# Optimization experiments

Measured on AMD Instinct MI355X. Metric: run time of the kernel, lower is better.

## Reference

```python
import jax, jax.numpy as jnp
import numpy as np

EPS = 1e-5  # torch BatchNorm2d default eps


def _lin(x, W, b):
    # torch nn.Linear: y = x @ W.T + b, W is [out, in]
    return jnp.einsum('...i,oi->...o', x, W) + b


def _bn(x, g, b):
    # BatchNorm2d in training mode: normalize per channel (last axis here)
    # over all other axes (B, N, K) with biased variance.
    m = jnp.mean(x, axis=(0, 1, 2), keepdims=True)
    v = jnp.mean(jnp.square(x - m), axis=(0, 1, 2), keepdims=True)
    return (x - m) * jax.lax.rsqrt(v + EPS) * g + b


def _gelu(x):
    return jax.nn.gelu(x, approximate=False)  # torch F.gelu default is erf


def _knn_idx(points, k):
    # squared euclidean pairwise distances, then k smallest per query
    pn = jnp.sum(points * points, axis=-1)  # [B,N]
    d2 = pn[:, :, None] + pn[:, None, :] - 2.0 * jnp.einsum('bnd,bmd->bnm', points, points)
    _, idx = jax.lax.top_k(-d2, k)  # [B,N,k], nearest first (includes self)
    return idx


def _gather(x, idx):
    # x: [B,N,D], idx: [B,N,K] -> [B,N,K,D]
    return jax.vmap(lambda a, i: a[i])(x, idx)


def setup_inputs() -> dict:
    key = jax.random.key(0)
    ks = jax.random.split(key, 20)
    B, N, Dp, Df, k = 2, 8192, 3, 128, 16

    def lin_params(kw, kb, din, dout):
        s = 1.0 / np.sqrt(din)
        W = jax.random.uniform(kw, (dout, din), jnp.float32, -s, s)
        b = jax.random.uniform(kb, (dout,), jnp.float32, -s, s)
        return W, b

    Wq, bq = lin_params(ks[0], ks[1], Df, Df)
    Wk, bk = lin_params(ks[2], ks[3], Df, Df)
    Wv, bv = lin_params(ks[4], ks[5], Df, Df)
    Wd1, bd1 = lin_params(ks[6], ks[7], Dp, Dp)
    Wd2, bd2 = lin_params(ks[8], ks[9], Dp, Df)
    Wg1, bg1 = lin_params(ks[10], ks[11], Df, Df)
    Wg2, bg2 = lin_params(ks[12], ks[13], Df, Df)

    return {
        'feats': jax.random.normal(ks[14], (B, N, Df), jnp.float32),
        'points': jax.random.normal(ks[15], (B, N, Dp), jnp.float32),
        'Wq': Wq, 'bq': bq, 'Wk': Wk, 'bk': bk, 'Wv': Wv, 'bv': bv,
        'Wd1': Wd1, 'bd1': bd1, 'Wd2': Wd2, 'bd2': bd2,
        'Wg1': Wg1, 'bg1': bg1, 'Wg2': Wg2, 'bg2': bg2,
        'gd': jnp.ones((Dp,), jnp.float32), 'betad': jnp.zeros((Dp,), jnp.float32),
        'gg1': jnp.ones((Df,), jnp.float32), 'betag1': jnp.zeros((Df,), jnp.float32),
        'gg2': jnp.ones((Df,), jnp.float32), 'betag2': jnp.zeros((Df,), jnp.float32),
        'k': 16,
    }


def reference(feats, points, Wq, bq, Wk, bk, Wv, bv, Wd1, bd1, Wd2, bd2,
              Wg1, bg1, Wg2, bg2, gd, betad, gg1, betag1, gg2, betag2, k):
    idx = _knn_idx(points, k)                     # [B,N,k]
    knn_feats = _gather(feats, idx)               # [B,N,k,Df]
    knn_points = _gather(points, idx)             # [B,N,k,Dp]

    pos = points[:, :, None, :] - knn_points      # [B,N,k,Dp]
    pos = _lin(pos, Wd1, bd1)
    pos = _gelu(_bn(pos, gd, betad))
    pos = _lin(pos, Wd2, bd2)                     # [B,N,k,Df]

    q = _lin(feats, Wq, bq)                       # [B,N,Df]
    key_t = _lin(knn_feats, Wk, bk)               # [B,N,k,Df]
    gamma = q[:, :, None, :] - key_t + pos
    gamma = _gelu(_bn(gamma, gg1, betag1))
    gamma = _lin(gamma, Wg1, bg1)
    gamma = _gelu(_bn(gamma, gg2, betag2))
    gamma = _lin(gamma, Wg2, bg2)

    rho = jax.nn.softmax(gamma, axis=-2)          # softmax over k neighbors
    value = _lin(knn_feats, Wv, bv) + pos
    return jnp.einsum('bnkd,bnkd->bnd', rho, value)
```

## Files before the change

### kernel.cpp

```cpp
#include <hip/hip_runtime.h>
#include <hip/hip_bf16.h>
#include <math.h>

#define NPTS 8192
#define STAT_CNT 262144.0f
#define BN_EPS 1e-5f

typedef __attribute__((__ext_vector_type__(8))) __bf16 bf16x8;
typedef __attribute__((__ext_vector_type__(4))) float f32x4;

#define SD_SUM 0
#define SD_SSQ 4
#define SD_SC 8
#define SD_SH 12
#define SG1_SC 16
#define SG1_SH 144
#define SG2_SC 272
#define SG2_SH 400
#define PG1 528
#define PG2 8720
#define STATS_FLOATS 16912

__device__ __forceinline__ unsigned short f2b(float x){
  unsigned u = __float_as_uint(x);
  return (unsigned short)((u + 0x7FFFu + ((u>>16)&1u)) >> 16);
}
__device__ __forceinline__ float b2f(unsigned short h){
  return __uint_as_float(((unsigned)h)<<16);
}
__device__ __forceinline__ float gelu_f(float x){
  return 0.5f*x*(1.0f + erff(x*0.70710678118654752440f));
}
__device__ __forceinline__ int swz(int row, int byteInRow){
  return row*256 + (byteInRow ^ ((row&7)<<4));
}
__device__ __forceinline__ float dist2f(float qx,float qy,float qz,float qpn,
                                        float x,float y,float z,float w){
  return (qpn + w) - 2.0f*fmaf(qx,x,fmaf(qy,y,qz*z));
}

#define MFMA16(a,b,c) __builtin_amdgcn_mfma_f32_16x16x32_bf16((a),(b),(c),0,0,0)

__device__ __forceinline__ bf16x8 ldsA8(const unsigned short* sA, int row, int k){
  return *(const bf16x8*)((const char*)sA + swz(row, k*2));
}
__device__ __forceinline__ bf16x8 ldW8(const unsigned short* W, int n, int k){
  return *(const bf16x8*)(W + n*128 + k);
}

__device__ __forceinline__ void gemm32(f32x4 acc[2][8], const unsigned short* sA,
                                       const unsigned short* W, int row0, int lane){
  int r = lane & 15, g = lane >> 4;
  #pragma unroll
  for (int ks=0; ks<4; ++ks){
    int k = ks*32 + g*8;
    bf16x8 a0 = ldsA8(sA, row0 + r, k);
    bf16x8 a1 = ldsA8(sA, row0 + 16 + r, k);
    #pragma unroll
    for (int nt=0; nt<8; ++nt){
      bf16x8 b = ldW8(W, nt*16 + r, k);
      acc[0][nt] = MFMA16(a0, b, acc[0][nt]);
      acc[1][nt] = MFMA16(a1, b, acc[1][nt]);
    }
  }
}

__global__ __launch_bounds__(256) void k_prep(
    const float* __restrict__ feats, const float* __restrict__ Wq, const float* __restrict__ Wk,
    const float* __restrict__ Wv, const float* __restrict__ Wg1, const float* __restrict__ Wg2,
    unsigned short* __restrict__ wbf, unsigned short* __restrict__ featb, float* __restrict__ stats)
{
  int i = blockIdx.x*256 + threadIdx.x;
  featb[i] = f2b(feats[i]);
  if (i < 16384){
    wbf[i]        = f2b(Wq[i]);
    wbf[16384+i]  = f2b(Wk[i]);
    wbf[32768+i]  = f2b(Wv[i]);
    wbf[49152+i]  = f2b(Wg1[i]);
    wbf[65536+i]  = f2b(Wg2[i]);
  }
  if (i < STATS_FLOATS) stats[i] = 0.f;
}

__global__ __launch_bounds__(256) void k_knn5(const float* __restrict__ points, int* __restrict__ idxb){
  __shared__ float svD[16][64];
  __shared__ int   svI[16][64];
  __shared__ int   svC[16];
  int tid = threadIdx.x;
  int wid = tid>>6, lane = tid&63;
  int blk = blockIdx.x;
  int b = (blk*16) >> 13;
  const float* cb = points + (size_t)b*NPTS*3;
  int qbase = blk*16 + wid*4;
  float qx[4],qy[4],qz[4],qpn[4],lmin[4],tq[4];
  #pragma unroll
  for (int q=0;q<4;++q){
    const float* qp = points + (size_t)(qbase+q)*3;
    qx[q]=qp[0]; qy[q]=qp[1]; qz[q]=qp[2];
    qpn[q]=fmaf(qz[q],qz[q],fmaf(qy[q],qy[q],qx[q]*qx[q]));
    lmin[q]=3.4e38f;
  }
  if (lane < 4) svC[wid*4+lane] = 0;
  #pragma unroll 4
  for (int s=0;s<128;++s){
    int p = s*64 + lane;
    const float* sp = cb + (size_t)p*3;
    float x=sp[0], y=sp[1], z=sp[2];
    float w = fmaf(z,z,fmaf(y,y,x*x));
    #pragma unroll
    for (int q=0;q<4;++q){
      float d = dist2f(qx[q],qy[q],qz[q],qpn[q], x,y,z,w);
      lmin[q] = fminf(lmin[q], d);
    }
  }
  #pragma unroll
  for (int q=0;q<4;++q){
    float v = lmin[q];
    #pragma unroll
    for (int k=2;k<=64;k<<=1){
      #pragma unroll
      for (int j=k>>1;j>=1;j>>=1){
        float o = __shfl_xor(v, j);
        bool keepmin = ((lane & j)==0) == ((lane & k)==0);
        v = keepmin ? fminf(v,o) : fmaxf(v,o);
      }
    }
    tq[q] = __shfl(v, 15);
  }
  #pragma unroll 2
  for (int s=0;s<128;++s){
    int p = s*64 + lane;
    const float* sp = cb + (size_t)p*3;
    float x=sp[0], y=sp[1], z=sp[2];
    float w = fmaf(z,z,fmaf(y,y,x*x));
    #pragma unroll
    for (int q=0;q<4;++q){
      float d = dist2f(qx[q],qy[q],qz[q],qpn[q], x,y,z,w);
      if (d <= tq[q]){
        int wq = wid*4+q;
        int slot = atomicAdd(&svC[wq], 1);
        if (slot < 64){ svD[wq][slot]=d; svI[wq][slot]=p; }
      }
    }
  }
  __syncthreads();
  #pragma unroll 1
  for (int q=0;q<4;++q){
    int wq = wid*4+q;
    int n = svC[wq]; n = (n>64)?64:n;
    float d = (lane<n)? svD[wq][lane] : 3.4e38f;
    int   ii = (lane<n)? svI[wq][lane] : 0x7fffffff;
    int rank = 0;
    #pragma unroll 4
    for (int j=0;j<n;++j){
      float od = svD[wq][j]; int oi = svI[wq][j];
      rank += ((od<d)||(od==d && oi<ii)) ? 1 : 0;
    }
    if (lane<n && rank<16) idxb[(size_t)(qbase+q)*16 + rank] = ii;
  }
}

__global__ __launch_bounds__(256) void k_dstats(const int* __restrict__ idxb,
    const float* __restrict__ points, const float* __restrict__ Wd1, const float* __restrict__ bd1,
    float* __restrict__ stats){
  __shared__ float sS[6];
  if (threadIdx.x < 6) sS[threadIdx.x]=0.f;
  __syncthreads();
  int qi = blockIdx.x*256 + threadIdx.x;
  int b = qi >> 13;
  const float* qp = points + (size_t)qi*3;
  float qx=qp[0],qy=qp[1],qz=qp[2];
  float w00=Wd1[0],w01=Wd1[1],w02=Wd1[2],w10=Wd1[3],w11=Wd1[4],w12=Wd1[5],w20=Wd1[6],w21=Wd1[7],w22=Wd1[8];
  float b0=bd1[0],b1=bd1[1],b2=bd1[2];
  float s0=0,s1=0,s2=0,q0=0,q1=0,q2=0;
  #pragma unroll
  for (int j=0;j<16;j++){
    int nb = idxb[(size_t)qi*16 + j];
    const float* np_ = points + (size_t)(b*NPTS + nb)*3;
    float dx=qx-np_[0], dy=qy-np_[1], dz=qz-np_[2];
    float t0 = fmaf(dz,w02,fmaf(dy,w01,dx*w00)) + b0;
    float t1 = fmaf(dz,w12,fmaf(dy,w11,dx*w10)) + b1;
    float t2 = fmaf(dz,w22,fmaf(dy,w21,dx*w20)) + b2;
    s0+=t0; s1+=t1; s2+=t2;
    q0=fmaf(t0,t0,q0); q1=fmaf(t1,t1,q1); q2=fmaf(t2,t2,q2);
  }
  atomicAdd(&sS[0],s0); atomicAdd(&sS[1],s1); atomicAdd(&sS[2],s2);
  atomicAdd(&sS[3],q0); atomicAdd(&sS[4],q1); atomicAdd(&sS[5],q2);
  __syncthreads();
  if (threadIdx.x < 3) atomicAdd(&stats[SD_SUM+threadIdx.x], sS[threadIdx.x]);
  else if (threadIdx.x < 6) atomicAdd(&stats[SD_SSQ+threadIdx.x-3], sS[threadIdx.x]);
}

__global__ void k_finalize(float* stats, int sumOff, int ssqOff, const float* __restrict__ gm,
                           const float* __restrict__ bt, int scOff, int shOff, int C){
  int c = blockIdx.x*64 + threadIdx.x;
  if (c >= C) return;
  float m = stats[sumOff+c] * (1.0f/STAT_CNT);
  float v = stats[ssqOff+c] * (1.0f/STAT_CNT) - m*m;
  v = fmaxf(v, 0.0f);
  float rs = rsqrtf(v + BN_EPS);
  float sc = gm[c]*rs;
  stats[scOff+c] = sc;
  stats[shOff+c] = fmaf(-m, sc, bt[c]);
}

__global__ void k_finalizeP(float* stats, int partOff, const float* __restrict__ gm,
                            const float* __restrict__ bt, int scOff, int shOff){
  int c = blockIdx.x*64 + threadIdx.x;
  float s=0.f, q=0.f;
  #pragma unroll 4
  for (int p=0;p<32;p++){
    s += stats[partOff + p*256 + c];
    q += stats[partOff + p*256 + 128 + c];
  }
  float m = s * (1.0f/STAT_CNT);
  float v = fmaxf(q*(1.0f/STAT_CNT) - m*m, 0.0f);
  float rs = rsqrtf(v + BN_EPS);
  float sc = gm[c]*rs;
  stats[scOff+c] = sc;
  stats[shOff+c] = fmaf(-m, sc, bt[c]);
}

__global__ __launch_bounds__(256) void k_qkv(
    const unsigned short* __restrict__ featb, const unsigned short* __restrict__ wbf,
    const float* __restrict__ bq, const float* __restrict__ bk, const float* __restrict__ bv,
    float* __restrict__ qout, unsigned short* __restrict__ kout, unsigned short* __restrict__ vout)
{
  __shared__ __align__(16) unsigned short sA[64*128];
  int tid = threadIdx.x;
  size_t row0g = (size_t)blockIdx.x*64;
  for (int t=tid; t<1024; t+=256){
    int row=t>>4, cc=t&15;
    uint4 v = *(const uint4*)(featb + (row0g+row)*128 + cc*8);
    *(uint4*)((char*)sA + swz(row, cc*16)) = v;
  }
  __syncthreads();
  int wid=tid>>6, lane=tid&63;
  int r=lane&15, g=lane>>4;
  int row0 = wid*16;
  f32x4 aQ[8]={}, aK[8]={}, aV[8]={};
  const unsigned short* WQ = wbf;
  const unsigned short* WK = wbf+16384;
  const unsigned short* WV = wbf+32768;
  #pragma unroll
  for (int ks=0;ks<4;++ks){
    int k = ks*32 + g*8;
    bf16x8 a0 = ldsA8(sA, row0+r, k);
    #pragma unroll
    for (int nt=0;nt<8;++nt){
      aQ[nt]=MFMA16(a0, ldW8(WQ,nt*16+r,k), aQ[nt]);
      aK[nt]=MFMA16(a0, ldW8(WK,nt*16+r,k), aK[nt]);
      aV[nt]=MFMA16(a0, ldW8(WV,nt*16+r,k), aV[nt]);
    }
  }
  #pragma unroll
  for (int nt=0;nt<8;++nt){
    int ch=nt*16+r;
    float bqc=bq[ch], bkc=bk[ch], bvc=bv[ch];
    #pragma unroll
    for (int rr=0;rr<4;++rr){
      size_t grow = row0g + row0 + g*4 + rr;
      qout[grow*128+ch] = aQ[nt][rr]+bqc;
      kout[grow*128+ch] = f2b(aK[nt][rr]+bkc);
      vout[grow*128+ch] = f2b(aV[nt][rr]+bvc);
    }
  }
}

__global__ __launch_bounds__(256) void k_fuse(
    const float* __restrict__ points, const int* __restrict__ idxb,
    const float* __restrict__ qbuf, const unsigned short* __restrict__ kb,
    const unsigned short* __restrict__ vb,
    const float* __restrict__ Wd1, const float* __restrict__ bd1,
    const float* __restrict__ Wd2, const float* __restrict__ bd2,
    float* __restrict__ stats,
    unsigned short* __restrict__ g1out, unsigned short* __restrict__ valout)
{
  __shared__ float sSum[128];
  __shared__ float sSq[128];
  int tid = threadIdx.x, blk = blockIdx.x;
  int slot = tid & 15, jg = tid >> 4;
  int lane = tid & 63;
  int ch0 = slot*8;
  if (tid < 128){ sSum[tid]=0.f; sSq[tid]=0.f; }
  float w2[24], b2v[8];
  #pragma unroll
  for (int u=0;u<8;++u){
    w2[u*3+0]=Wd2[(ch0+u)*3+0];
    w2[u*3+1]=Wd2[(ch0+u)*3+1];
    w2[u*3+2]=Wd2[(ch0+u)*3+2];
    b2v[u]=bd2[ch0+u];
  }
  int c = slot & 3; c = (c==3)?2:c;
  float wa  = (c==0)?Wd1[0]:((c==1)?Wd1[3]:Wd1[6]);
  float wb_ = (c==0)?Wd1[1]:((c==1)?Wd1[4]:Wd1[7]);
  float wc  = (c==0)?Wd1[2]:((c==1)?Wd1[5]:Wd1[8]);
  float bc_ = (c==0)?bd1[0]:((c==1)?bd1[1]:bd1[2]);
  float sc_ = (c==0)?stats[SD_SC+0]:((c==1)?stats[SD_SC+1]:stats[SD_SC+2]);
  float sh_ = (c==0)?stats[SD_SH+0]:((c==1)?stats[SD_SH+1]:stats[SD_SH+2]);
  int base = lane & 48;
  float accS[8]={0,0,0,0,0,0,0,0}, accQ[8]={0,0,0,0,0,0,0,0};
  __syncthreads();
  #pragma unroll 2
  for (int i=0;i<8;++i){
    int q = blk*8 + i;
    int b = q >> 13;
    int row = q*16 + jg;
    int nb = idxb[row];
    const float* ctr = points + (size_t)q*3;
    const float* np_ = points + (size_t)(b*NPTS + nb)*3;
    float dx = ctr[0]-np_[0], dy = ctr[1]-np_[1], dz = ctr[2]-np_[2];
    float t = fmaf(dz, wc, fmaf(dy, wb_, dx*wa)) + bc_;
    float tc = gelu_f(fmaf(t, sc_, sh_));
    float g0  = __shfl(tc, base+0);
    float g1v = __shfl(tc, base+1);
    float g2v = __shfl(tc, base+2);
    size_t kvoff = ((size_t)(b*NPTS + nb))*128 + ch0;
    union { uint4 u; unsigned short s[8]; } K, V, G, Vo;
    K.u = *(const uint4*)(kb + kvoff);
    V.u = *(const uint4*)(vb + kvoff);
    float4 q0 = *(const float4*)(qbuf + (size_t)q*128 + ch0);
    float4 q1 = *(const float4*)(qbuf + (size_t)q*128 + ch0 + 4);
    float qv[8] = {q0.x,q0.y,q0.z,q0.w,q1.x,q1.y,q1.z,q1.w};
    #pragma unroll
    for (int u=0;u<8;++u){
      float pos = fmaf(g2v, w2[u*3+2], fmaf(g1v, w2[u*3+1], g0*w2[u*3+0])) + b2v[u];
      float key = b2f(K.s[u]);
      float val = b2f(V.s[u]) + pos;
      float gmv = qv[u] - key + pos;
      accS[u] += gmv; accQ[u] = fmaf(gmv,gmv,accQ[u]);
      G.s[u] = f2b(gmv); Vo.s[u] = f2b(val);
    }
    *(uint4*)(g1out + (size_t)row*128 + ch0) = G.u;
    *(uint4*)(valout + (size_t)row*128 + ch0) = Vo.u;
  }
  #pragma unroll
  for (int u=0;u<8;++u){
    atomicAdd(&sSum[ch0+u], accS[u]);
    atomicAdd(&sSq[ch0+u], accQ[u]);
  }
  __syncthreads();
  if (tid < 128){
    int ps = blk & 31;
    atomicAdd(&stats[PG1 + ps*256 + tid], sSum[tid]);
    atomicAdd(&stats[PG1 + ps*256 + 128 + tid], sSq[tid]);
  }
}

__global__ __launch_bounds__(256) void k_g(
    const unsigned short* __restrict__ gin, const unsigned short* __restrict__ W,
    const float* __restrict__ bias, float* __restrict__ stats, int scOff, int shOff,
    unsigned short* __restrict__ gout, int partOff)
{
  __shared__ __align__(16) unsigned short sA[128*128];
  __shared__ float sSum[128];
  __shared__ float sSq[128];
  int tid = threadIdx.x;
  size_t row0 = (size_t)blockIdx.x*128;
  if (tid<128){ sSum[tid]=0.f; sSq[tid]=0.f; }
  for (int t=tid; t<2048; t+=256){
    int row=t>>4, c=t&15;
    union { uint4 u; unsigned short s[8]; } iv, ov;
    iv.u = *(const uint4*)(gin + (row0+row)*128 + c*8);
    #pragma unroll
    for (int u=0;u<8;u++){
      int ch = c*8+u;
      float x = b2f(iv.s[u]);
      x = gelu_f(fmaf(x, stats[scOff+ch], stats[shOff+ch]));
      ov.s[u] = f2b(x);
    }
    *(uint4*)((char*)sA + swz(row, c*16)) = ov.u;
  }
  __syncthreads();
  int wid=tid>>6, lane=tid&63;
  int r=lane&15, g=lane>>4;
  f32x4 acc[2][8] = {};
  gemm32(acc, sA, W, wid*32, lane);
  #pragma unroll
  for (int nt=0;nt<8;++nt){
    int ch = nt*16+r;
    float bc = bias[ch];
    float s_=0.f, qq=0.f;
    #pragma unroll
    for (int mt=0;mt<2;++mt){
      #pragma unroll
      for (int rr=0;rr<4;++rr){
        int row = wid*32 + mt*16 + g*4 + rr;
        float x = acc[mt][nt][rr] + bc;
        s_ += x; qq = fmaf(x,x,qq);
        gout[(row0+row)*128 + ch] = f2b(x);
      }
    }
    atomicAdd(&sSum[ch], s_); atomicAdd(&sSq[ch], qq);
  }
  __syncthreads();
  if (tid<128){
    int slot = blockIdx.x & 31;
    atomicAdd(&stats[partOff + slot*256 + tid], sSum[tid]);
    atomicAdd(&stats[partOff + slot*256 + 128 + tid], sSq[tid]);
  }
}

__global__ __launch_bounds__(256) void k_out(
    const unsigned short* __restrict__ gin, const unsigned short* __restrict__ W,
    const float* __restrict__ bias, const float* __restrict__ stats, int scOff, int shOff,
    const unsigned short* __restrict__ val, float* __restrict__ outp)
{
  __shared__ __align__(16) unsigned short sA[128*128];
  __shared__ __align__(16) unsigned short sV[128*128];
  int tid=threadIdx.x;
  size_t row0=(size_t)blockIdx.x*128;
  for (int t=tid;t<2048;t+=256){
    int row=t>>4,c=t&15;
    union { uint4 u; unsigned short s[8]; } iv, ov;
    iv.u = *(const uint4*)(gin + (row0+row)*128 + c*8);
    #pragma unroll
    for (int u=0;u<8;u++){
      int ch=c*8+u;
      float x = b2f(iv.s[u]);
      x = gelu_f(fmaf(x, stats[scOff+ch], stats[shOff+ch]));
      ov.s[u]=f2b(x);
    }
    *(uint4*)((char*)sA + swz(row,c*16)) = ov.u;
    uint4 vv = *(const uint4*)(val + (row0+row)*128 + c*8);
    *(uint4*)((char*)sV + swz(row,c*16)) = vv;
  }
  __syncthreads();
  int wid=tid>>6, lane=tid&63;
  int r=lane&15, g=lane>>4;
  f32x4 acc[2][8] = {};
  gemm32(acc, sA, W, wid*32, lane);
  #pragma unroll
  for (int nt=0;nt<8;++nt){
    int ch=nt*16+r; float bc=bias[ch];
    #pragma unroll
    for (int mt=0;mt<2;++mt){
      float g3[4], vv[4];
      #pragma unroll
      for (int rr=0;rr<4;++rr){
        int row=wid*32+mt*16+g*4+rr;
        g3[rr]=acc[mt][nt][rr]+bc;
        vv[rr]=b2f(*(const unsigned short*)((const char*)sV + swz(row, ch*2)));
      }
      float m = fmaxf(fmaxf(g3[0],g3[1]),fmaxf(g3[2],g3[3]));
      m = fmaxf(m, __shfl_xor(m,16));
      m = fmaxf(m, __shfl_xor(m,32));
      float s=0.f, o=0.f;
      #pragma unroll
      for (int rr=0;rr<4;++rr){
        float e = __expf(g3[rr]-m);
        s += e; o = fmaf(e, vv[rr], o);
      }
      s += __shfl_xor(s,16); s += __shfl_xor(s,32);
      o += __shfl_xor(o,16); o += __shfl_xor(o,32);
      if (g==0){
        int p = wid*2+mt;
        outp[((size_t)blockIdx.x*8 + p)*128 + ch] = o/s;
      }
    }
  }
}

extern "C" void kernel_launch(void* const* d_in, const int* in_sizes, int n_in,
                              void* d_out, int out_size, void* d_ws, size_t ws_size,
                              hipStream_t stream)
{
  const float* feats  = (const float*)d_in[0];
  const float* points = (const float*)d_in[1];
  const float* Wq = (const float*)d_in[2];  const float* bq = (const float*)d_in[3];
  const float* Wk = (const float*)d_in[4];  const float* bk = (const float*)d_in[5];
  const float* Wv = (const float*)d_in[6];  const float* bv = (const float*)d_in[7];
  const float* Wd1= (const float*)d_in[8];  const float* bd1= (const float*)d_in[9];
  const float* Wd2= (const float*)d_in[10]; const float* bd2= (const float*)d_in[11];
  const float* Wg1= (const float*)d_in[12]; const float* bg1= (const float*)d_in[13];
  const float* Wg2= (const float*)d_in[14]; const float* bg2= (const float*)d_in[15];
  const float* gd = (const float*)d_in[16]; const float* betad = (const float*)d_in[17];
  const float* gg1= (const float*)d_in[18]; const float* betag1= (const float*)d_in[19];
  const float* gg2= (const float*)d_in[20]; const float* betag2= (const float*)d_in[21];
  float* outp = (float*)d_out;

  char* ws = (char*)d_ws;
  int*    idxb  = (int*)   (ws + 0);
  float*  stats = (float*) (ws + 1048576);
  unsigned short* wbf   = (unsigned short*)(ws + 1179648);
  unsigned short* featb = (unsigned short*)(ws + 1343488);
  unsigned short* kb    = (unsigned short*)(ws + 5537792);
  unsigned short* vbuf  = (unsigned short*)(ws + 9732096);
  unsigned short* g1b = (unsigned short*)(ws + 13926400);
  unsigned short* vab = (unsigned short*)(ws + 81035264);
  unsigned short* g2b = (unsigned short*)(ws + 148144128);
  float*  qbuf  = (float*) (ws + 215252992);

  k_prep<<<dim3(8192),dim3(256),0,stream>>>(feats,Wq,Wk,Wv,Wg1,Wg2,wbf,featb,stats);
  k_knn5<<<dim3(1024),dim3(256),0,stream>>>(points,idxb);
  k_dstats<<<dim3(64),dim3(256),0,stream>>>(idxb,points,Wd1,bd1,stats);
  k_finalize<<<dim3(1),dim3(64),0,stream>>>(stats,SD_SUM,SD_SSQ,gd,betad,SD_SC,SD_SH,3);
  k_qkv<<<dim3(256),dim3(256),0,stream>>>(featb,wbf,bq,bk,bv,qbuf,kb,vbuf);
  k_fuse<<<dim3(2048),dim3(256),0,stream>>>(points,idxb,qbuf,kb,vbuf,Wd1,bd1,Wd2,bd2,stats,g1b,vab);
  k_finalizeP<<<dim3(2),dim3(64),0,stream>>>(stats,PG1,gg1,betag1,SG1_SC,SG1_SH);
  k_g<<<dim3(2048),dim3(256),0,stream>>>(g1b,wbf+49152,bg1,stats,SG1_SC,SG1_SH,g2b,PG2);
  k_finalizeP<<<dim3(2),dim3(64),0,stream>>>(stats,PG2,gg2,betag2,SG2_SC,SG2_SH);
  k_out<<<dim3(2048),dim3(256),0,stream>>>(g2b,wbf+65536,bg2,stats,SG2_SC,SG2_SH,vab,outp);
  (void)in_sizes; (void)n_in; (void)out_size; (void)ws_size;
}
```

Before: 376.5 us.

## Halve row tiles in k_g/k_out and approximate erf-based GELU with polynomial

Swaps the erff-based GELU for an Abramowitz-Stegun polynomial erf approximation that uses __expf, which is cheaper than the library erf. It also shrinks the k_g and k_out tiles from 128 to 64 rows per block, with one 16-row MFMA tile per wave, and doubles the grid. Smaller tiles cut LDS use and accumulator registers, which should raise occupancy, at the cost of reading the weights from global memory twice as often. The erf approximation has an error of about 1e-7, which is fine given the bf16 storage, so it is not a hack.

```diff
diff --git a/kernel.cpp b/kernel.cpp
--- a/kernel.cpp
+++ b/kernel.cpp
@@ -29,7 +29,12 @@
   return __uint_as_float(((unsigned)h)<<16);
 }
 __device__ __forceinline__ float gelu_f(float x){
-  return 0.5f*x*(1.0f + erff(x*0.70710678118654752440f));
+  float u = fabsf(x)*0.70710678118654752440f;
+  float t = 1.0f/fmaf(0.3275911f, u, 1.0f);
+  float p = t*fmaf(t,fmaf(t,fmaf(t,fmaf(t,1.061405429f,-1.453152027f),1.421413741f),-0.284496736f),0.254829592f);
+  float er = fmaf(-p, __expf(-u*u), 1.0f);
+  er = (x < 0.f) ? -er : er;
+  return 0.5f*x*(1.0f+er);
 }
 __device__ __forceinline__ int swz(int row, int byteInRow){
   return row*256 + (byteInRow ^ ((row&7)<<4));
@@ -46,23 +51,6 @@
 }
 __device__ __forceinline__ bf16x8 ldW8(const unsigned short* W, int n, int k){
   return *(const bf16x8*)(W + n*128 + k);
-}
-
-__device__ __forceinline__ void gemm32(f32x4 acc[2][8], const unsigned short* sA,
-                                       const unsigned short* W, int row0, int lane){
-  int r = lane & 15, g = lane >> 4;
-  #pragma unroll
-  for (int ks=0; ks<4; ++ks){
-    int k = ks*32 + g*8;
-    bf16x8 a0 = ldsA8(sA, row0 + r, k);
-    bf16x8 a1 = ldsA8(sA, row0 + 16 + r, k);
-    #pragma unroll
-    for (int nt=0; nt<8; ++nt){
-      bf16x8 b = ldW8(W, nt*16 + r, k);
-      acc[0][nt] = MFMA16(a0, b, acc[0][nt]);
-      acc[1][nt] = MFMA16(a1, b, acc[1][nt]);
-    }
-  }
 }
 
 __global__ __launch_bounds__(256) void k_prep(
@@ -352,13 +340,13 @@
     const float* __restrict__ bias, float* __restrict__ stats, int scOff, int shOff,
     unsigned short* __restrict__ gout, int partOff)
 {
-  __shared__ __align__(16) unsigned short sA[128*128];
+  __shared__ __align__(16) unsigned short sA[64*128];
   __shared__ float sSum[128];
   __shared__ float sSq[128];
   int tid = threadIdx.x;
-  size_t row0 = (size_t)blockIdx.x*128;
+  size_t row0 = (size_t)blockIdx.x*64;
   if (tid<128){ sSum[tid]=0.f; sSq[tid]=0.f; }
-  for (int t=tid; t<2048; t+=256){
+  for (int t=tid; t<1024; t+=256){
     int row=t>>4, c=t&15;
     union { uint4 u; unsigned short s[8]; } iv, ov;
     iv.u = *(const uint4*)(gin + (row0+row)*128 + c*8);
@@ -374,22 +362,27 @@
   __syncthreads();
   int wid=tid>>6, lane=tid&63;
   int r=lane&15, g=lane>>4;
-  f32x4 acc[2][8] = {};
-  gemm32(acc, sA, W, wid*32, lane);
+  int row0l = wid*16;
+  f32x4 acc[8] = {};
+  #pragma unroll
+  for (int ks=0;ks<4;++ks){
+    int k = ks*32 + g*8;
+    bf16x8 a0 = ldsA8(sA, row0l+r, k);
+    #pragma unroll
+    for (int nt=0;nt<8;++nt)
+      acc[nt] = MFMA16(a0, ldW8(W,nt*16+r,k), acc[nt]);
+  }
   #pragma unroll
   for (int nt=0;nt<8;++nt){
     int ch = nt*16+r;
     float bc = bias[ch];
     float s_=0.f, qq=0.f;
     #pragma unroll
-    for (int mt=0;mt<2;++mt){
-      #pragma unroll
-      for (int rr=0;rr<4;++rr){
-        int row = wid*32 + mt*16 + g*4 + rr;
-        float x = acc[mt][nt][rr] + bc;
-        s_ += x; qq = fmaf(x,x,qq);
-        gout[(row0+row)*128 + ch] = f2b(x);
-      }
+    for (int rr=0;rr<4;++rr){
+      int row = row0l + g*4 + rr;
+      float x = acc[nt][rr] + bc;
+      s_ += x; qq = fmaf(x,x,qq);
+      gout[(row0+row)*128 + ch] = f2b(x);
     }
     atomicAdd(&sSum[ch], s_); atomicAdd(&sSq[ch], qq);
   }
@@ -406,11 +399,11 @@
     const float* __restrict__ bias, const float* __restrict__ stats, int scOff, int shOff,
     const unsigned short* __restrict__ val, float* __restrict__ outp)
 {
-  __shared__ __align__(16) unsigned short sA[128*128];
-  __shared__ __align__(16) unsigned short sV[128*128];
+  __shared__ __align__(16) unsigned short sA[64*128];
+  __shared__ __align__(16) unsigned short sV[64*128];
   int tid=threadIdx.x;
-  size_t row0=(size_t)blockIdx.x*128;
-  for (int t=tid;t<2048;t+=256){
+  size_t row0=(size_t)blockIdx.x*64;
+  for (int t=tid;t<1024;t+=256){
     int row=t>>4,c=t&15;
     union { uint4 u; unsigned short s[8]; } iv, ov;
     iv.u = *(const uint4*)(gin + (row0+row)*128 + c*8);
@@ -428,35 +421,39 @@
   __syncthreads();
   int wid=tid>>6, lane=tid&63;
   int r=lane&15, g=lane>>4;
-  f32x4 acc[2][8] = {};
-  gemm32(acc, sA, W, wid*32, lane);
+  int row0l = wid*16;
+  f32x4 acc[8] = {};
+  #pragma unroll
+  for (int ks=0;ks<4;++ks){
+    int k = ks*32 + g*8;
+    bf16x8 a0 = ldsA8(sA, row0l+r, k);
+    #pragma unroll
+    for (int nt=0;nt<8;++nt)
+      acc[nt] = MFMA16(a0, ldW8(W,nt*16+r,k), acc[nt]);
+  }
   #pragma unroll
   for (int nt=0;nt<8;++nt){
     int ch=nt*16+r; float bc=bias[ch];
-    #pragma unroll
-    for (int mt=0;mt<2;++mt){
-      float g3[4], vv[4];
-      #pragma unroll
-      for (int rr=0;rr<4;++rr){
-        int row=wid*32+mt*16+g*4+rr;
-        g3[rr]=acc[mt][nt][rr]+bc;
-        vv[rr]=b2f(*(const unsigned short*)((const char*)sV + swz(row, ch*2)));
-      }
-      float m = fmaxf(fmaxf(g3[0],g3[1]),fmaxf(g3[2],g3[3]));
-      m = fmaxf(m, __shfl_xor(m,16));
-      m = fmaxf(m, __shfl_xor(m,32));
-      float s=0.f, o=0.f;
-      #pragma unroll
-      for (int rr=0;rr<4;++rr){
-        float e = __expf(g3[rr]-m);
-        s += e; o = fmaf(e, vv[rr], o);
-      }
-      s += __shfl_xor(s,16); s += __shfl_xor(s,32);
-      o += __shfl_xor(o,16); o += __shfl_xor(o,32);
-      if (g==0){
-        int p = wid*2+mt;
-        outp[((size_t)blockIdx.x*8 + p)*128 + ch] = o/s;
-      }
+    float g3[4], vv[4];
+    #pragma unroll
+    for (int rr=0;rr<4;++rr){
+      int row=row0l+g*4+rr;
+      g3[rr]=acc[nt][rr]+bc;
+      vv[rr]=b2f(*(const unsigned short*)((const char*)sV + swz(row, ch*2)));
+    }
+    float m = fmaxf(fmaxf(g3[0],g3[1]),fmaxf(g3[2],g3[3]));
+    m = fmaxf(m, __shfl_xor(m,16));
+    m = fmaxf(m, __shfl_xor(m,32));
+    float s=0.f, o=0.f;
+    #pragma unroll
+    for (int rr=0;rr<4;++rr){
+      float e = __expf(g3[rr]-m);
+      s += e; o = fmaf(e, vv[rr], o);
+    }
+    s += __shfl_xor(s,16); s += __shfl_xor(s,32);
+    o += __shfl_xor(o,16); o += __shfl_xor(o,32);
+    if (g==0){
+      outp[((size_t)blockIdx.x*4 + wid)*128 + ch] = o/s;
     }
   }
 }
@@ -498,8 +495,8 @@
   k_qkv<<<dim3(256),dim3(256),0,stream>>>(featb,wbf,bq,bk,bv,qbuf,kb,vbuf);
   k_fuse<<<dim3(2048),dim3(256),0,stream>>>(points,idxb,qbuf,kb,vbuf,Wd1,bd1,Wd2,bd2,stats,g1b,vab);
   k_finalizeP<<<dim3(2),dim3(64),0,stream>>>(stats,PG1,gg1,betag1,SG1_SC,SG1_SH);
-  k_g<<<dim3(2048),dim3(256),0,stream>>>(g1b,wbf+49152,bg1,stats,SG1_SC,SG1_SH,g2b,PG2);
+  k_g<<<dim3(4096),dim3(256),0,stream>>>(g1b,wbf+49152,bg1,stats,SG1_SC,SG1_SH,g2b,PG2);
   k_finalizeP<<<dim3(2),dim3(64),0,stream>>>(stats,PG2,gg2,betag2,SG2_SC,SG2_SH);
-  k_out<<<dim3(2048),dim3(256),0,stream>>>(g2b,wbf+65536,bg2,stats,SG2_SC,SG2_SH,vab,outp);
+  k_out<<<dim3(4096),dim3(256),0,stream>>>(g2b,wbf+65536,bg2,stats,SG2_SC,SG2_SH,vab,outp);
   (void)in_sizes; (void)n_in; (void)out_size; (void)ws_size;
 }
```

Result: slower. 409.8 us (+8.8%).
